# Performance work log

Hardware: AMD Instinct MI355X
Metric: run time of the kernel (lower is better)

## Reference

```python
import jax, jax.numpy as jnp
import numpy as np

T, B, D, H = 2048, 32, 512, 512


def setup_inputs() -> dict:
    key = jax.random.key(0)
    k0, k1, k2, k3 = jax.random.split(key, 4)
    inp = jax.random.normal(k0, (T, B, D), dtype=jnp.float32) * 0.1
    paddings = (jax.random.uniform(k1, (T, B, 1)) > 0.9).astype(jnp.float32)
    W_x = jax.random.normal(k2, (D, 4 * H), dtype=jnp.float32) / np.sqrt(D)
    W_h = jax.random.normal(k3, (H, 4 * H), dtype=jnp.float32) / np.sqrt(H)
    b = jnp.zeros((4 * H,), dtype=jnp.float32)
    return {"input": inp, "paddings": paddings, "W_x": W_x, "W_h": W_h, "b": b}


def reference(input, paddings, W_x, W_h, b):
    """Masked LSTM recurrence over time.

    input:    [T, B, D]
    paddings: [T, B, 1] (1.0 = padded -> carry previous state)
    returns (outputs [T, B, H], (m [B, H], c [B, H]))
    """
    batch = input.shape[1]
    m0 = jnp.zeros((batch, H), dtype=input.dtype)
    c0 = jnp.zeros((batch, H), dtype=input.dtype)

    # Precompute input projections for all timesteps in one big GEMM.
    x_proj = jnp.einsum('tbd,dk->tbk', input, W_x) + b  # [T, B, 4H]

    def step(carry, xt_pt):
        m, c = carry
        xp, p = xt_pt                      # xp: [B, 4H], p: [B, 1]
        gates = xp + m @ W_h               # [B, 4H]
        i, f, g, o = jnp.split(gates, 4, axis=-1)
        c_new = jax.nn.sigmoid(f) * c + jax.nn.sigmoid(i) * jnp.tanh(g)
        m_new = jax.nn.sigmoid(o) * jnp.tanh(c_new)
        m2 = m_new * (1.0 - p) + m * p
        c2 = c_new * (1.0 - p) + c * p
        return (m2, c2), m2

    (m_f, c_f), outputs = jax.lax.scan(step, (m0, c0), (x_proj, paddings))
    return outputs, (m_f, c_f)
```

## Files before the change

kernel.cpp:

```cpp
#include <hip/hip_runtime.h>


typedef __bf16  bf16x8 __attribute__((ext_vector_type(8)));
typedef float   f32x4  __attribute__((ext_vector_type(4)));

__device__ __forceinline__ unsigned short f2bf(float f) {
  unsigned u = __builtin_bit_cast(unsigned, f);
  u += 0x7fffu + ((u >> 16) & 1u);
  return (unsigned short)(u >> 16);
}
__device__ __forceinline__ float bf2f(unsigned short h) {
  unsigned u = ((unsigned)h) << 16;
  return __builtin_bit_cast(float, u);
}
__device__ __forceinline__ float fast_sigmoid(float x) {
  return __builtin_amdgcn_rcpf(1.0f + __expf(-x));
}
__device__ __forceinline__ float fast_tanh(float x) {
  return 2.0f * __builtin_amdgcn_rcpf(1.0f + __expf(-2.0f * x)) - 1.0f;
}

__global__ __launch_bounds__(256) void transpose_cvt(
    const float* __restrict__ Wx, const float* __restrict__ Wh,
    unsigned short* __restrict__ WxT, unsigned short* __restrict__ WhT) {
  const float* src = blockIdx.z ? Wh : Wx;
  unsigned short* dst = blockIdx.z ? WhT : WxT;
  __shared__ float tile[32][33];
  const int n0 = blockIdx.x * 32, k0 = blockIdx.y * 32;
  const int t = threadIdx.x;
  {
    const int kk = t >> 3, nn = (t & 7) * 4;
    float4 v = *(const float4*)(src + (size_t)(k0 + kk) * 2048 + n0 + nn);
    tile[kk][nn + 0] = v.x; tile[kk][nn + 1] = v.y;
    tile[kk][nn + 2] = v.z; tile[kk][nn + 3] = v.w;
  }
  __syncthreads();
  {
    const int n = t >> 3, k4 = (t & 7) * 4;
    ushort4 o;
    o.x = f2bf(tile[k4 + 0][n]); o.y = f2bf(tile[k4 + 1][n]);
    o.z = f2bf(tile[k4 + 2][n]); o.w = f2bf(tile[k4 + 3][n]);
    *(ushort4*)(dst + (size_t)(n0 + n) * 512 + k0 + k4) = o;
  }
}

__global__ __launch_bounds__(256) void gemm_xproj(
    const float* __restrict__ A, const unsigned short* __restrict__ BT,
    const float* __restrict__ bias, unsigned short* __restrict__ C) {
  __shared__ unsigned short As[128 * 32];
  __shared__ unsigned short Bs[128 * 32];
  const int m0 = blockIdx.x * 128, n0 = blockIdx.y * 128;
  const int tid = threadIdx.x, w = tid >> 6, lane = tid & 63;
  const int q = lane >> 4, r = lane & 15;
  const int wm = (w >> 1) * 64, wn = (w & 1) * 64;
  const int srow = tid >> 1, shalf = tid & 1;

  f32x4 acc[4][4] = {};

  for (int kt = 0; kt < 16; ++kt) {
    const int k0 = kt * 32;
    {
      const float* ap = A + (size_t)(m0 + srow) * 512 + k0 + shalf * 16;
#pragma unroll
      for (int c = 0; c < 4; ++c) {
        float4 v = *(const float4*)(ap + c * 4);
        ushort4 h;
        h.x = f2bf(v.x); h.y = f2bf(v.y); h.z = f2bf(v.z); h.w = f2bf(v.w);
        *(ushort4*)&As[srow * 32 + shalf * 16 + c * 4] = h;
      }
    }
    {
      const unsigned short* bp = BT + (size_t)(n0 + srow) * 512 + k0 + shalf * 16;
#pragma unroll
      for (int c2 = 0; c2 < 2; ++c2)
        *(uint4*)&Bs[srow * 32 + shalf * 16 + c2 * 8] = *(const uint4*)(bp + c2 * 8);
    }
    __syncthreads();
    bf16x8 af[4], bfr[4];
#pragma unroll
    for (int i = 0; i < 4; ++i)
      af[i] = *(const bf16x8*)&As[(wm + i * 16 + r) * 32 + q * 8];
#pragma unroll
    for (int j = 0; j < 4; ++j)
      bfr[j] = *(const bf16x8*)&Bs[(wn + j * 16 + r) * 32 + q * 8];
#pragma unroll
    for (int i = 0; i < 4; ++i)
#pragma unroll
      for (int j = 0; j < 4; ++j)
        acc[i][j] = __builtin_amdgcn_mfma_f32_16x16x32_bf16(af[i], bfr[j], acc[i][j], 0, 0, 0);
    __syncthreads();
  }
#pragma unroll
  for (int j = 0; j < 4; ++j) {
    const int col = n0 + wn + j * 16 + r;
    const float bv = bias[col];
#pragma unroll
    for (int i = 0; i < 4; ++i) {
#pragma unroll
      for (int e = 0; e < 4; ++e) {
        const int row = m0 + wm + i * 16 + q * 4 + e;
        C[(size_t)row * 2048 + col] = f2bf(acc[i][j][e] + bv);
      }
    }
  }
}

__global__ __launch_bounds__(256, 1) void lstm_rec(
    const unsigned short* __restrict__ xp,
    const float* __restrict__ pads,
    const unsigned short* __restrict__ WhT,
    float* __restrict__ out,
    unsigned* __restrict__ tb,
    unsigned* __restrict__ slots) {
  const int g = blockIdx.x, tid = threadIdx.x;
  const int w = tid >> 6, lane = tid & 63, q = lane >> 4, r = lane & 15;

  __shared__ unsigned mAv[2 * 8192];
  __shared__ float gsm[64 * 33];

  const int n_loc = w * 16 + r;
  const int h_loc = n_loc >> 2, typ = n_loc & 3;
  const int n_glob = typ * 512 + g * 16 + h_loc;
  bf16x8 bfrag[16];
#pragma unroll
  for (int kt = 0; kt < 16; ++kt)
    bfrag[kt] = *(const bf16x8*)(WhT + (size_t)n_glob * 512 + kt * 32 + q * 8);

  const int row = lane >> 1;
  const int hglob = g * 16 + w * 4 + (lane & 1) * 2;
  const unsigned mwoff = (unsigned)((hglob >> 5) * 2 + (row >> 4)) * 1024u +
                         (unsigned)(((hglob >> 3) & 3) * 16 + (row & 15)) * 16u +
                         (unsigned)(hglob & 7) * 2u;
  unsigned* const pub = (unsigned*)((char*)tb + mwoff);
  unsigned* const spoll = slots + (lane & 31) * 16;
  float cst0 = 0.f, cst1 = 0.f, mst0 = 0.f, mst1 = 0.f;

  float pf_p = pads[row];
  unsigned pf_x[4];
#pragma unroll
  for (int ty = 0; ty < 4; ++ty)
    pf_x[ty] = *(const unsigned*)(xp + (size_t)row * 2048 + ty * 512 + hglob);

  for (int t = 0; t < 2048; ++t) {
    const unsigned* mr = tb + (size_t)(t & 1) * 8192;
    unsigned mt[32];
#pragma unroll
    for (int i = 0; i < 32; ++i)
      mt[i] = __hip_atomic_load(mr + i * 256 + tid, __ATOMIC_RELAXED,
                                __HIP_MEMORY_SCOPE_AGENT);
    unsigned* dsd = &mAv[(t & 1) * 8192];
#pragma unroll
    for (int i = 0; i < 32; ++i)
      dsd[i * 256 + tid] = mt[i];
    asm volatile("s_waitcnt lgkmcnt(0)" ::: "memory");
    __builtin_amdgcn_sched_barrier(0);
    __builtin_amdgcn_s_barrier();
    __builtin_amdgcn_sched_barrier(0);

    const char* mbase = (const char*)&mAv[(t & 1) * 8192];
    f32x4 a00 = {}, a01 = {}, a10 = {}, a11 = {};
#pragma unroll
    for (int kt = 0; kt < 16; kt += 2) {
      bf16x8 a0 = *(const bf16x8*)(mbase + (size_t)(kt * 2 + 0) * 1024 + lane * 16);
      bf16x8 a1 = *(const bf16x8*)(mbase + (size_t)(kt * 2 + 1) * 1024 + lane * 16);
      a00 = __builtin_amdgcn_mfma_f32_16x16x32_bf16(a0, bfrag[kt], a00, 0, 0, 0);
      a10 = __builtin_amdgcn_mfma_f32_16x16x32_bf16(a1, bfrag[kt], a10, 0, 0, 0);
      bf16x8 a2 = *(const bf16x8*)(mbase + (size_t)(kt * 2 + 2) * 1024 + lane * 16);
      bf16x8 a3 = *(const bf16x8*)(mbase + (size_t)(kt * 2 + 3) * 1024 + lane * 16);
      a01 = __builtin_amdgcn_mfma_f32_16x16x32_bf16(a2, bfrag[kt + 1], a01, 0, 0, 0);
      a11 = __builtin_amdgcn_mfma_f32_16x16x32_bf16(a3, bfrag[kt + 1], a11, 0, 0, 0);
    }
    const f32x4 acc0 = a00 + a01, acc1 = a10 + a11;

#pragma unroll
    for (int e = 0; e < 4; ++e) {
      gsm[n_loc * 33 + q * 4 + e]      = acc0[e];
      gsm[n_loc * 33 + 16 + q * 4 + e] = acc1[e];
    }
    const float* gcol = gsm + (size_t)(w * 16 + (lane & 1) * 8) * 33 + row;
    float gt[8];
#pragma unroll
    for (int j = 0; j < 8; ++j) gt[j] = gcol[j * 33];

    const float p = pf_p;
    const float xi0 = bf2f((unsigned short)(pf_x[0] & 0xffff));
    const float xi1 = bf2f((unsigned short)(pf_x[0] >> 16));
    const float xf0 = bf2f((unsigned short)(pf_x[1] & 0xffff));
    const float xf1 = bf2f((unsigned short)(pf_x[1] >> 16));
    const float xg0 = bf2f((unsigned short)(pf_x[2] & 0xffff));
    const float xg1 = bf2f((unsigned short)(pf_x[2] >> 16));
    const float xo0 = bf2f((unsigned short)(pf_x[3] & 0xffff));
    const float xo1 = bf2f((unsigned short)(pf_x[3] >> 16));

    const float si0 = fast_sigmoid(gt[0] + xi0), sf0 = fast_sigmoid(gt[1] + xf0);
    const float tg0 = fast_tanh(gt[2] + xg0),    so0 = fast_sigmoid(gt[3] + xo0);
    const float si1 = fast_sigmoid(gt[4] + xi1), sf1 = fast_sigmoid(gt[5] + xf1);
    const float tg1 = fast_tanh(gt[6] + xg1),    so1 = fast_sigmoid(gt[7] + xo1);

    const float cn0 = sf0 * cst0 + si0 * tg0;
    const float cn1 = sf1 * cst1 + si1 * tg1;
    const float mn0 = so0 * fast_tanh(cn0);
    const float mn1 = so1 * fast_tanh(cn1);
    const float m20 = mn0 + p * (mst0 - mn0), c20 = cn0 + p * (cst0 - cn0);
    const float m21 = mn1 + p * (mst1 - mn1), c21 = cn1 + p * (cst1 - cn1);
    cst0 = c20; mst0 = m20; cst1 = c21; mst1 = m21;

    unsigned vpoll = 0;
    if (t < 2047) {
      const unsigned pack = (unsigned)f2bf(m20) | ((unsigned)f2bf(m21) << 16);
      __hip_atomic_store(pub + (size_t)((t + 1) & 1) * 8192, pack,
                         __ATOMIC_RELAXED, __HIP_MEMORY_SCOPE_AGENT);
      asm volatile("s_waitcnt vmcnt(0)" ::: "memory");
      __builtin_amdgcn_sched_barrier(0);
      __builtin_amdgcn_s_barrier();
      if (tid == 0)
        __hip_atomic_store(slots + g * 16, (unsigned)(t + 1),
                           __ATOMIC_RELAXED, __HIP_MEMORY_SCOPE_AGENT);
      vpoll = __hip_atomic_load(spoll, __ATOMIC_RELAXED,
                                __HIP_MEMORY_SCOPE_AGENT);
    }

    *(float2*)(out + (size_t)t * 16384 + (size_t)row * 512 + hglob) =
        make_float2(m20, m21);

    if (t < 2047) {
      pf_p = pads[(t + 1) * 32 + row];
#pragma unroll
      for (int ty = 0; ty < 4; ++ty)
        pf_x[ty] = *(const unsigned*)(xp + (size_t)((t + 1) * 32 + row) * 2048 + ty * 512 + hglob);

      const unsigned tgt = (unsigned)(t + 1);
      for (;;) {
        if (__ballot(vpoll < tgt) == 0ull) break;
        __builtin_amdgcn_s_sleep(1);
        vpoll = __hip_atomic_load(spoll, __ATOMIC_RELAXED,
                                  __HIP_MEMORY_SCOPE_AGENT);
      }
    }
  }

  {
    float* mo = out + 33554432 + (size_t)row * 512 + hglob;
    *(float2*)mo = make_float2(mst0, mst1);
    *(float2*)(mo + 16384) = make_float2(cst0, cst1);
  }
}

extern "C" void kernel_launch(void* const* d_in, const int* in_sizes, int n_in,
                              void* d_out, int out_size, void* d_ws, size_t ws_size,
                              hipStream_t stream) {
  (void)in_sizes; (void)n_in; (void)out_size; (void)ws_size;
  const float* input = (const float*)d_in[0];
  const float* pads  = (const float*)d_in[1];
  const float* Wx    = (const float*)d_in[2];
  const float* Wh    = (const float*)d_in[3];
  const float* bias  = (const float*)d_in[4];
  float* out = (float*)d_out;

  char* ws = (char*)d_ws;
  unsigned short* xp  = (unsigned short*)(ws);
  unsigned short* WxT = (unsigned short*)(ws + 268435456);
  unsigned short* WhT = (unsigned short*)(ws + 270532608);
  unsigned* tb        = (unsigned*)(ws + 272629760);
  unsigned* slots     = (unsigned*)(ws + 272695296);

  hipMemsetAsync(ws + 272629760, 0, 65536 + 2048, stream);

  transpose_cvt<<<dim3(64, 16, 2), 256, 0, stream>>>(Wx, Wh, WxT, WhT);
  gemm_xproj<<<dim3(512, 16), 256, 0, stream>>>(input, WxT, bias, xp);
  lstm_rec<<<32, 256, 0, stream>>>(xp, pads, WhT, out, tb, slots);
}
```

Measured before the change: 7.268 ms.

## Fuse input-projection GEMM into persistent LSTM kernel with per-chunk readiness flags

Replaces the separate x-projection GEMM launch with a single persistent kernel of 256 blocks. 32 blocks run the recurrence while the other 224 compute GEMM tiles in time order and bump per-chunk counters. The recurrent blocks wait on those counters before loading each group of 8 timesteps. The aim is to hide the GEMM time behind the serial recurrence. The cost is extra atomic traffic and polling, plus the risk that the GEMM blocks compete for bandwidth or fall behind the recurrence.

```diff
diff --git a/kernel.cpp b/kernel.cpp
--- a/kernel.cpp
+++ b/kernel.cpp
@@ -44,79 +44,92 @@
   }
 }
 
-__global__ __launch_bounds__(256) void gemm_xproj(
-    const float* __restrict__ A, const unsigned short* __restrict__ BT,
-    const float* __restrict__ bias, unsigned short* __restrict__ C) {
-  __shared__ unsigned short As[128 * 32];
-  __shared__ unsigned short Bs[128 * 32];
-  const int m0 = blockIdx.x * 128, n0 = blockIdx.y * 128;
-  const int tid = threadIdx.x, w = tid >> 6, lane = tid & 63;
-  const int q = lane >> 4, r = lane & 15;
-  const int wm = (w >> 1) * 64, wn = (w & 1) * 64;
-  const int srow = tid >> 1, shalf = tid & 1;
-
-  f32x4 acc[4][4] = {};
-
-  for (int kt = 0; kt < 16; ++kt) {
-    const int k0 = kt * 32;
-    {
-      const float* ap = A + (size_t)(m0 + srow) * 512 + k0 + shalf * 16;
-#pragma unroll
-      for (int c = 0; c < 4; ++c) {
-        float4 v = *(const float4*)(ap + c * 4);
-        ushort4 h;
-        h.x = f2bf(v.x); h.y = f2bf(v.y); h.z = f2bf(v.z); h.w = f2bf(v.w);
-        *(ushort4*)&As[srow * 32 + shalf * 16 + c * 4] = h;
-      }
-    }
-    {
-      const unsigned short* bp = BT + (size_t)(n0 + srow) * 512 + k0 + shalf * 16;
-#pragma unroll
-      for (int c2 = 0; c2 < 2; ++c2)
-        *(uint4*)&Bs[srow * 32 + shalf * 16 + c2 * 8] = *(const uint4*)(bp + c2 * 8);
-    }
-    __syncthreads();
-    bf16x8 af[4], bfr[4];
-#pragma unroll
-    for (int i = 0; i < 4; ++i)
-      af[i] = *(const bf16x8*)&As[(wm + i * 16 + r) * 32 + q * 8];
-#pragma unroll
-    for (int j = 0; j < 4; ++j)
-      bfr[j] = *(const bf16x8*)&Bs[(wn + j * 16 + r) * 32 + q * 8];
-#pragma unroll
-    for (int i = 0; i < 4; ++i)
-#pragma unroll
-      for (int j = 0; j < 4; ++j)
-        acc[i][j] = __builtin_amdgcn_mfma_f32_16x16x32_bf16(af[i], bfr[j], acc[i][j], 0, 0, 0);
-    __syncthreads();
-  }
-#pragma unroll
-  for (int j = 0; j < 4; ++j) {
-    const int col = n0 + wn + j * 16 + r;
-    const float bv = bias[col];
-#pragma unroll
-    for (int i = 0; i < 4; ++i) {
-#pragma unroll
-      for (int e = 0; e < 4; ++e) {
-        const int row = m0 + wm + i * 16 + q * 4 + e;
-        C[(size_t)row * 2048 + col] = f2bf(acc[i][j][e] + bv);
-      }
-    }
-  }
-}
-
-__global__ __launch_bounds__(256, 1) void lstm_rec(
-    const unsigned short* __restrict__ xp,
+__global__ __launch_bounds__(256, 1) void lstm_fused(
+    const float* __restrict__ input,
+    const unsigned short* __restrict__ WxT,
+    const float* __restrict__ bias,
+    unsigned short* __restrict__ xp,
     const float* __restrict__ pads,
     const unsigned short* __restrict__ WhT,
     float* __restrict__ out,
     unsigned* __restrict__ tb,
     unsigned* __restrict__ slots) {
-  const int g = blockIdx.x, tid = threadIdx.x;
+  const int bid = blockIdx.x, tid = threadIdx.x;
   const int w = tid >> 6, lane = tid & 63, q = lane >> 4, r = lane & 15;
 
   __shared__ unsigned mAv[2 * 8192];
   __shared__ float gsm[64 * 33];
+
+  if (bid >= 32) {
+    unsigned short* As = (unsigned short*)mAv;
+    unsigned short* Bs = (unsigned short*)(mAv + 2048);
+    const int wm = (w >> 1) * 64, wn = (w & 1) * 64;
+    const int srow = tid >> 1, shalf = tid & 1;
+    for (int tile = bid - 32; tile < 8192; tile += 224) {
+      const int m0 = (tile >> 4) * 128, n0 = (tile & 15) * 128;
+      f32x4 acc[4][4] = {};
+      for (int kt = 0; kt < 16; ++kt) {
+        const int k0 = kt * 32;
+        {
+          const float* ap = input + (size_t)(m0 + srow) * 512 + k0 + shalf * 16;
+#pragma unroll
+          for (int c = 0; c < 4; ++c) {
+            float4 v = *(const float4*)(ap + c * 4);
+            ushort4 h;
+            h.x = f2bf(v.x); h.y = f2bf(v.y); h.z = f2bf(v.z); h.w = f2bf(v.w);
+            *(ushort4*)&As[srow * 32 + shalf * 16 + c * 4] = h;
+          }
+        }
+        {
+          const unsigned short* bp = WxT + (size_t)(n0 + srow) * 512 + k0 + shalf * 16;
+#pragma unroll
+          for (int c2 = 0; c2 < 2; ++c2)
+            *(uint4*)&Bs[srow * 32 + shalf * 16 + c2 * 8] = *(const uint4*)(bp + c2 * 8);
+        }
+        __syncthreads();
+        bf16x8 af[4], bfr[4];
+#pragma unroll
+        for (int i = 0; i < 4; ++i)
+          af[i] = *(const bf16x8*)&As[(wm + i * 16 + r) * 32 + q * 8];
+#pragma unroll
+        for (int j = 0; j < 4; ++j)
+          bfr[j] = *(const bf16x8*)&Bs[(wn + j * 16 + r) * 32 + q * 8];
+#pragma unroll
+        for (int i = 0; i < 4; ++i)
+#pragma unroll
+          for (int j = 0; j < 4; ++j)
+            acc[i][j] = __builtin_amdgcn_mfma_f32_16x16x32_bf16(af[i], bfr[j], acc[i][j], 0, 0, 0);
+        __syncthreads();
+      }
+#pragma unroll
+      for (int j = 0; j < 4; ++j) {
+        const int col = n0 + wn + j * 16 + r;
+        const float bv = bias[col];
+#pragma unroll
+        for (int i = 0; i < 4; ++i) {
+#pragma unroll
+          for (int e = 0; e < 4; ++e) {
+            const int row = m0 + wm + i * 16 + q * 4 + e;
+            const unsigned u = (unsigned)f2bf(acc[i][j][e] + bv);
+            const unsigned hi = (unsigned)__shfl_down((int)u, 1);
+            if ((r & 1) == 0)
+              __hip_atomic_store((unsigned*)(xp + (size_t)row * 2048 + col),
+                                 u | (hi << 16), __ATOMIC_RELAXED,
+                                 __HIP_MEMORY_SCOPE_AGENT);
+          }
+        }
+      }
+      asm volatile("s_waitcnt vmcnt(0)" ::: "memory");
+      __syncthreads();
+      if (tid == 0) {
+        const int fm = tile >> 5;
+        atomicAdd(&slots[(fm >> 3) * 16 + 8 + (fm & 7)], 1u);
+      }
+    }
+    return;
+  }
+
+  const int g = bid;
 
   const int n_loc = w * 16 + r;
   const int h_loc = n_loc >> 2, typ = n_loc & 3;
@@ -135,11 +148,21 @@
   unsigned* const spoll = slots + (lane & 31) * 16;
   float cst0 = 0.f, cst1 = 0.f, mst0 = 0.f, mst1 = 0.f;
 
+  for (;;) {
+    unsigned fv = __hip_atomic_load(slots + 8, __ATOMIC_RELAXED,
+                                    __HIP_MEMORY_SCOPE_AGENT);
+    if (fv >= 32u) break;
+    __builtin_amdgcn_s_sleep(1);
+  }
+  asm volatile("" ::: "memory");
   float pf_p = pads[row];
   unsigned pf_x[4];
 #pragma unroll
   for (int ty = 0; ty < 4; ++ty)
-    pf_x[ty] = *(const unsigned*)(xp + (size_t)row * 2048 + ty * 512 + hglob);
+    pf_x[ty] = __hip_atomic_load(
+        (const unsigned*)(xp + (size_t)row * 2048 + ty * 512 + hglob),
+        __ATOMIC_RELAXED, __HIP_MEMORY_SCOPE_AGENT);
+  int wmreg = 1;
 
   for (int t = 0; t < 2048; ++t) {
     const unsigned* mr = tb + (size_t)(t & 1) * 8192;
@@ -224,10 +247,24 @@
         make_float2(m20, m21);
 
     if (t < 2047) {
+      const int fn = (t + 1) >> 3;
+      if (fn >= wmreg) {
+        unsigned* fpp = slots + ((fn >> 3) * 16 + 8 + (fn & 7));
+        for (;;) {
+          unsigned fv = __hip_atomic_load(fpp, __ATOMIC_RELAXED,
+                                          __HIP_MEMORY_SCOPE_AGENT);
+          if (fv >= 32u) break;
+          __builtin_amdgcn_s_sleep(1);
+        }
+        asm volatile("" ::: "memory");
+        wmreg = fn + 1;
+      }
       pf_p = pads[(t + 1) * 32 + row];
 #pragma unroll
       for (int ty = 0; ty < 4; ++ty)
-        pf_x[ty] = *(const unsigned*)(xp + (size_t)((t + 1) * 32 + row) * 2048 + ty * 512 + hglob);
+        pf_x[ty] = __hip_atomic_load(
+            (const unsigned*)(xp + (size_t)((t + 1) * 32 + row) * 2048 + ty * 512 + hglob),
+            __ATOMIC_RELAXED, __HIP_MEMORY_SCOPE_AGENT);
 
       const unsigned tgt = (unsigned)(t + 1);
       for (;;) {
@@ -267,6 +304,6 @@
   hipMemsetAsync(ws + 272629760, 0, 65536 + 2048, stream);
 
   transpose_cvt<<<dim3(64, 16, 2), 256, 0, stream>>>(Wx, Wh, WxT, WhT);
-  gemm_xproj<<<dim3(512, 16), 256, 0, stream>>>(input, WxT, bias, xp);
-  lstm_rec<<<32, 256, 0, stream>>>(xp, pads, WhT, out, tb, slots);
-}
+  lstm_fused<<<256, 256, 0, stream>>>(input, WxT, bias, xp, pads, WhT, out,
+                                      tb, slots);
+}
```

After: 7.470 ms. +2.8%, slower.
